# Kernel tuning notes

Hardware: AMD Instinct MI355X
Metric: run time of the kernel (lower is better)

## Reference

```python
import jax, jax.numpy as jnp
import numpy as np

EMBED_DIM = 1024
B, S = 4, 2048
SCALE = float(np.sqrt(EMBED_DIM))


def setup_inputs() -> dict:
    key = jax.random.key(0)
    ks = jax.random.split(key, 9)
    d = EMBED_DIM
    init = 1.0 / np.sqrt(d)
    return {
        "query": jax.random.normal(ks[0], (B, S, d), jnp.float32),
        "key": jax.random.normal(ks[1], (B, S, d), jnp.float32),
        "value": jax.random.normal(ks[2], (B, S, d), jnp.float32),
        "wq": jax.random.uniform(ks[3], (d, d), jnp.float32, -init, init),
        "bq": jax.random.uniform(ks[4], (d,), jnp.float32, -init, init),
        "wk": jax.random.uniform(ks[5], (d, d), jnp.float32, -init, init),
        "bk": jax.random.uniform(ks[6], (d,), jnp.float32, -init, init),
        "wv": jax.random.uniform(ks[7], (d, d), jnp.float32, -init, init),
        "bv": jax.random.uniform(ks[8], (d,), jnp.float32, -init, init),
    }


def reference(query, key, value, wq, bq, wk, bk, wv, bv):
    # Linear projections (torch Linear: x @ W^T + b; here weights stored as [in, out])
    q = query @ wq + bq            # [B,S,D]
    k = key @ wk + bk              # [B,S,D]
    v = value @ wv + bv            # [B,S,D]
    scores = jnp.einsum("bqd,bkd->bqk", q, k) / SCALE   # [B,S,S]
    attn = jax.nn.softmax(scores, axis=-1)
    # dropout in eval mode -> identity
    return jnp.einsum("bqk,bkd->bqd", attn, v)          # [B,S,D]
```

## Files before the change

kernel.cpp:

```cpp
#include <hip/hip_runtime.h>
#include <hip/hip_bf16.h>

typedef __attribute__((ext_vector_type(4))) float   f32x4;
typedef __attribute__((ext_vector_type(8))) __bf16  bf16x8;
typedef __attribute__((ext_vector_type(4))) __bf16  bf16x4;

#define NB 4
#define SS 2048
#define DD 1024

__device__ __forceinline__ void gload_lds16(const void* g, void* l) {
  __builtin_amdgcn_global_load_lds((const __attribute__((address_space(1))) void*)g,
                                   (__attribute__((address_space(3))) void*)l,
                                   16, 0, 0);
}

__global__ __launch_bounds__(256) void prep_kernel(
    const float* __restrict__ q, const float* __restrict__ k, const float* __restrict__ v,
    const float* __restrict__ wq, const float* __restrict__ wk, const float* __restrict__ wv,
    const float* __restrict__ bq, const float* __restrict__ bk, const float* __restrict__ bv,
    __bf16* __restrict__ X, __bf16* __restrict__ Wt, float* __restrict__ biasbuf)
{
  const int z = blockIdx.z;
  __shared__ float t[32][33];
  if (blockIdx.x < 8192) {
    const float* src = z == 0 ? q : (z == 1 ? k : v);
    __bf16* dst = X + (size_t)z * (size_t)(NB * SS * DD);
    size_t i = ((size_t)blockIdx.x * 256 + threadIdx.x) * 4;
    float4 f = *(const float4*)&src[i];
    bf16x4 o = { (__bf16)f.x, (__bf16)f.y, (__bf16)f.z, (__bf16)f.w };
    *(bf16x4*)&dst[i] = o;
  } else {
    const int idx = blockIdx.x - 8192;
    const float* W  = z == 0 ? wq : (z == 1 ? wk : wv);
    const float* bi = z == 0 ? bq : (z == 1 ? bk : bv);
    __bf16* dst = Wt + (size_t)z * (size_t)(DD * DD);
    const int n0 = (idx & 31) * 32, k0 = (idx >> 5) * 32;
    const int tx = threadIdx.x & 31, ty = threadIdx.x >> 5;
    #pragma unroll
    for (int i = 0; i < 4; i++)
      t[ty + 8 * i][tx] = W[(size_t)(k0 + ty + 8 * i) * DD + n0 + tx];
    __syncthreads();
    #pragma unroll
    for (int i = 0; i < 4; i++)
      dst[(size_t)(n0 + ty + 8 * i) * DD + k0 + tx] = (__bf16)t[tx][ty + 8 * i];
    if (idx == 0) {
      #pragma unroll
      for (int i = 0; i < 4; i++)
        biasbuf[z * DD + threadIdx.x + 256 * i] = bi[threadIdx.x + 256 * i];
    }
  }
}


#define G2A(BUF) ((BUF) * 16384)
#define G2B(BUF) (32768 + (BUF) * 16384)

#define G2_STAGE(BUF, T) do { int t_ = (((T) + koff) & (NT - 1));               \
  const __bf16* gA_ = Ablk + (size_t)t_ * 64;                                   \
  const __bf16* gB_ = Bblk + (size_t)t_ * 64;                                   \
  gload_lds16(gA_ + o0, smem + G2A(BUF) + tid * 16);                            \
  gload_lds16(gA_ + o1, smem + G2A(BUF) + 4096 + tid * 16);                     \
  gload_lds16(gA_ + o2, smem + G2A(BUF) + 8192 + tid * 16);                     \
  gload_lds16(gA_ + o3, smem + G2A(BUF) + 12288 + tid * 16);                    \
  gload_lds16(gB_ + o0, smem + G2B(BUF) + tid * 16);                            \
  gload_lds16(gB_ + o1, smem + G2B(BUF) + 4096 + tid * 16);                     \
  gload_lds16(gB_ + o2, smem + G2B(BUF) + 8192 + tid * 16);                     \
  gload_lds16(gB_ + o3, smem + G2B(BUF) + 12288 + tid * 16); } while (0)

template <int EPI>
__global__ __launch_bounds__(256, 2) void gemm2b_kernel(
    const __bf16* __restrict__ A, const __bf16* __restrict__ B,
    const float* __restrict__ bias, float* __restrict__ Fout,
    __bf16* __restrict__ Qo, __bf16* __restrict__ Ko, __bf16* __restrict__ Vt,
    int K, int lda, int ldb, int ldc,
    long strideA, long strideB, long strideC)
{
  extern __shared__ char smem[];

  const int gx = gridDim.x, gy = gridDim.y;
  const int nwg = gx * gy * gridDim.z;
  int lin = blockIdx.x + gx * (blockIdx.y + gy * blockIdx.z);
  const int cpx = nwg >> 3;
  int swz = (lin & 7) * cpx + (lin >> 3);
  const int bx = swz % gx;
  int rem = swz / gx;
  const int by = rem % gy;
  const int bz = rem / gy;

  const long brow = (long)by * 128, bcol = (long)bx * 128;
  const __bf16* Ablk = A + (size_t)bz * strideA + (size_t)brow * lda;
  const __bf16* Bblk = B + (size_t)bz * strideB + (size_t)bcol * ldb;

  const int tid  = threadIdx.x;
  const int lane = tid & 63;
  const int wid  = tid >> 6;
  const int wm = wid >> 1, wn = wid & 1;
  const int l15 = lane & 15, l4 = lane >> 4;
  const int lx = (lane & 7) << 4;

  const int NT = K >> 6;
  const int koff = (blockIdx.x & 1) * (NT >> 1);

  int o0, o1, o2, o3;
  #pragma unroll
  for (int i = 0; i < 4; ++i) {
    const int p = i * 4096 + tid * 16;
    const int r = p >> 7;
    const int kb = (p ^ ((r & 7) << 4)) & 127;
    const int off = r * lda + (kb >> 1);
    if (i == 0) o0 = off; else if (i == 1) o1 = off;
    else if (i == 2) o2 = off; else o3 = off;
  }

  int ara[2], brb[2];
  #pragma unroll
  for (int ks = 0; ks < 2; ++ks) {
    ara[ks] = ((((wm * 64 + l15) * 64 + l4 * 8) * 2) + ks * 64) ^ lx;
    brb[ks] = ((((wn * 64 + l15) * 64 + l4 * 8) * 2) + ks * 64) ^ lx;
  }

  f32x4 acc[4][4] = {};
  f32x4 accs[4] = {};
  bf16x8 af[4][2], bf[4][2];
  bf16x8 onesf;
  #pragma unroll
  for (int j = 0; j < 8; ++j) onesf[j] = (__bf16)1.0f;

  G2_STAGE(0, 0);
  G2_STAGE(1, 1);
  asm volatile("s_waitcnt vmcnt(8)" ::: "memory");
  __builtin_amdgcn_s_barrier();

  for (int t = 0; t < NT; ++t) {
    const int cur = t & 1;
    const int abase = cur * 16384;
    const int bbase = 32768 + cur * 16384;
    #pragma unroll
    for (int mi = 0; mi < 4; ++mi)
      #pragma unroll
      for (int ks = 0; ks < 2; ++ks)
        af[mi][ks] = *(const bf16x8*)(smem + abase + ara[ks] + mi * 2048);
    #pragma unroll
    for (int ni = 0; ni < 4; ++ni)
      #pragma unroll
      for (int ks = 0; ks < 2; ++ks)
        bf[ni][ks] = *(const bf16x8*)(smem + bbase + brb[ks] + ni * 2048);
    asm volatile("s_waitcnt lgkmcnt(0)" ::: "memory");
    __builtin_amdgcn_sched_barrier(0);
    __builtin_amdgcn_s_barrier();
    G2_STAGE(cur, t + 2);
    __builtin_amdgcn_s_setprio(1);
    #pragma unroll
    for (int mi = 0; mi < 4; ++mi)
      #pragma unroll
      for (int ni = 0; ni < 4; ++ni)
        #pragma unroll
        for (int ks = 0; ks < 2; ++ks)
          acc[mi][ni] = __builtin_amdgcn_mfma_f32_16x16x32_bf16(
              af[mi][ks], bf[ni][ks], acc[mi][ni], 0, 0, 0);
    if constexpr (EPI == 2) {
      #pragma unroll
      for (int mi = 0; mi < 4; ++mi)
        #pragma unroll
        for (int ks = 0; ks < 2; ++ks)
          accs[mi] = __builtin_amdgcn_mfma_f32_16x16x32_bf16(
              af[mi][ks], onesf, accs[mi], 0, 0, 0);
    }
    __builtin_amdgcn_s_setprio(0);
    __builtin_amdgcn_sched_barrier(0);
    asm volatile("s_waitcnt vmcnt(8)" ::: "memory");
    __builtin_amdgcn_s_barrier();
  }

  if constexpr (EPI == 2) {
    float* C = Fout + (size_t)bz * strideC;
    #pragma unroll
    for (int mi = 0; mi < 4; ++mi) {
      f32x4 inv;
      #pragma unroll
      for (int e = 0; e < 4; ++e) inv[e] = 1.0f / accs[mi][e];
      #pragma unroll
      for (int ni = 0; ni < 4; ++ni) {
        const long row = brow + wm * 64 + mi * 16 + l4 * 4;
        const long col = bcol + wn * 64 + ni * 16 + l15;
        #pragma unroll
        for (int e = 0; e < 4; ++e)
          C[(row + e) * (size_t)ldc + col] = acc[mi][ni][e] * inv[e];
      }
    }
  } else {
    if (bz == 2) {
      #pragma unroll
      for (int mi = 0; mi < 4; ++mi) {
        #pragma unroll
        for (int ni = 0; ni < 4; ++ni) {
          const long row = brow + wm * 64 + mi * 16 + l4 * 4;
          const long col = bcol + wn * 64 + ni * 16 + l15;
          const float bvv = bias[2 * DD + col];
          const long bb = row >> 11, s = row & 2047;
          bf16x4 pk = { (__bf16)(acc[mi][ni][0] + bvv), (__bf16)(acc[mi][ni][1] + bvv),
                        (__bf16)(acc[mi][ni][2] + bvv), (__bf16)(acc[mi][ni][3] + bvv) };
          *(bf16x4*)&Vt[bb * 2097152 + col * 2048 + s] = pk;
        }
      }
    } else {
      __bf16* C = bz == 0 ? Qo : Ko;
      #pragma unroll
      for (int mi = 0; mi < 4; ++mi) {
        #pragma unroll
        for (int ni = 0; ni < 4; ++ni) {
          const long row = brow + wm * 64 + mi * 16 + l4 * 4;
          const long col = bcol + wn * 64 + ni * 16 + l15;
          const float bvv = bias[bz * DD + col];
          #pragma unroll
          for (int e = 0; e < 4; ++e)
            C[(row + e) * 1024 + col] = (__bf16)(acc[mi][ni][e] + bvv);
        }
      }
    }
  }
}


#define A_OFF(BUF, MH) (((BUF)*2 + (MH)) * 16384)
#define B_OFF(BUF, NH) (65536 + ((BUF)*2 + (NH)) * 16384)

#define STAGE_A(BUF, MH, T) do { int t_ = (T); if (t_ >= NT) t_ = 0;            \
  const __bf16* gs_ = Ablk + (size_t)(MH) * (64 * (size_t)lda) + (size_t)t_ * 64; \
  gload_lds16(gs_ + aoff0, smem + A_OFF(BUF, MH) + tid * 16);                    \
  gload_lds16(gs_ + aoff1, smem + A_OFF(BUF, MH) + 8192 + tid * 16); } while (0)

#define STAGE_B(BUF, NH, T) do { int t_ = (T); if (t_ >= NT) t_ = 0;            \
  const __bf16* gs_ = Bblk + (size_t)(NH) * (32 * (size_t)ldb) + (size_t)t_ * 64; \
  gload_lds16(gs_ + boff0, smem + B_OFF(BUF, NH) + tid * 16);                    \
  gload_lds16(gs_ + boff1, smem + B_OFF(BUF, NH) + 8192 + tid * 16); } while (0)

#define DSREAD_A(DST, BUF, MH)                                                  \
  _Pragma("unroll") for (int mi = 0; mi < 4; ++mi) {                            \
    _Pragma("unroll") for (int ks = 0; ks < 2; ++ks)                            \
      DST[mi][ks] = *(const bf16x8*)(smem + A_OFF(BUF, MH) + arb[ks] + mi * 2048); }

#define DSREAD_BS(DST, BUF, NH)                                                 \
  _Pragma("unroll") for (int ni = 0; ni < 2; ++ni) {                            \
    _Pragma("unroll") for (int ks = 0; ks < 2; ++ks)                            \
      DST[ni][ks] = *(const bf16x8*)(smem + B_OFF(BUF, NH) + brb[ks] + ni * 2048); }

#define BARRIER_MFMA(AF, BF, MH, NH) do {                                       \
  __builtin_amdgcn_s_barrier();                                                 \
  asm volatile("s_waitcnt lgkmcnt(0)" ::: "memory");                            \
  __builtin_amdgcn_sched_barrier(0);                                            \
  __builtin_amdgcn_s_setprio(1);                                                \
  _Pragma("unroll") for (int mi = 0; mi < 4; ++mi)                              \
  _Pragma("unroll") for (int ni = 0; ni < 2; ++ni)                              \
  _Pragma("unroll") for (int ks = 0; ks < 2; ++ks)                              \
    acc[(MH)*4+mi][(NH)*2+ni] = __builtin_amdgcn_mfma_f32_16x16x32_bf16(        \
        AF[mi][ks], BF[ni][ks], acc[(MH)*4+mi][(NH)*2+ni], 0, 0, 0);            \
  __builtin_amdgcn_s_setprio(0);                                                \
  __builtin_amdgcn_sched_barrier(0);                                            \
  __builtin_amdgcn_s_barrier(); } while (0)

__global__ __launch_bounds__(512) void gemm8p_kernel(
    const __bf16* __restrict__ A, const __bf16* __restrict__ B,
    float scale, void* __restrict__ Cout,
    int K, int lda, int ldb, int ldc,
    long strideA, long strideB, long strideC)
{
  extern __shared__ char smem[];

  const int gx = gridDim.x, gy = gridDim.y;
  const int nwg = gx * gy * gridDim.z;
  int lin = blockIdx.x + gx * (blockIdx.y + gy * blockIdx.z);
  const int cpx = nwg >> 3;
  int swz = (lin & 7) * cpx + (lin >> 3);
  const int bx = swz % gx;
  int rem = swz / gx;
  const int by = rem % gy;
  const int bz = rem / gy;

  const long brow = (long)by * 256, bcol = (long)bx * 256;
  const __bf16* Ablk = A + (size_t)bz * strideA + (size_t)brow * lda;
  const __bf16* Bblk = B + (size_t)bz * strideB + (size_t)bcol * ldb;

  const int tid  = threadIdx.x;
  const int lane = tid & 63;
  const int wid  = tid >> 6;
  const int wm = wid >> 2, wn = wid & 3;
  const int l15 = lane & 15, l4 = lane >> 4;
  const int lx = (lane & 7) << 4;

  const int NT = K >> 6;
  const int niter = NT >> 1;

  int aoff0, aoff1, boff0, boff1;
  #pragma unroll
  for (int i = 0; i < 2; ++i) {
    const int p = i * 8192 + tid * 16;
    const int l = p ^ (((p >> 7) & 7) << 4);
    const int r = p >> 7;
    const int kb = l & 127;
    const int av = ((r >> 6) * 128 + (r & 63)) * lda + (kb >> 1);
    const int bv = ((r >> 5) * 64 + (r & 31)) * ldb + (kb >> 1);
    if (i == 0) { aoff0 = av; boff0 = bv; } else { aoff1 = av; boff1 = bv; }
  }

  int arb[2], brb[2];
  #pragma unroll
  for (int ks = 0; ks < 2; ++ks) {
    arb[ks] = ((((wm * 64 + l15) * 64 + l4 * 8) * 2) + ks * 64) ^ lx;
    brb[ks] = ((((wn * 32 + l15) * 64 + l4 * 8) * 2) + ks * 64) ^ lx;
  }

  f32x4 acc[8][4] = {};
  bf16x8 a0[4][2], a1[4][2], b0[2][2], b1[2][2];

  STAGE_B(0, 0, 0); STAGE_A(0, 0, 0); STAGE_A(0, 1, 0); STAGE_B(0, 1, 0);
  STAGE_B(1, 0, 1); STAGE_A(1, 0, 1);
  asm volatile("s_waitcnt vmcnt(4)" ::: "memory");
  __builtin_amdgcn_s_barrier();

  for (int it = 0; it < niter; ++it) {
    const int tt = it * 2;
    DSREAD_A(a0, 0, 0); DSREAD_BS(b0, 0, 0);
    STAGE_A(1, 1, tt + 1);
    BARRIER_MFMA(a0, b0, 0, 0);
    DSREAD_A(a1, 0, 1);
    STAGE_B(1, 1, tt + 1);
    BARRIER_MFMA(a1, b0, 1, 0);
    DSREAD_BS(b1, 0, 1);
    STAGE_B(0, 0, tt + 2);
    BARRIER_MFMA(a0, b1, 0, 1);
    STAGE_A(0, 0, tt + 2);
    asm volatile("s_waitcnt vmcnt(4)" ::: "memory");
    BARRIER_MFMA(a1, b1, 1, 1);
    DSREAD_A(a0, 1, 0); DSREAD_BS(b0, 1, 0);
    STAGE_A(0, 1, tt + 2);
    BARRIER_MFMA(a0, b0, 0, 0);
    DSREAD_A(a1, 1, 1);
    STAGE_B(0, 1, tt + 2);
    BARRIER_MFMA(a1, b0, 1, 0);
    DSREAD_BS(b1, 1, 1);
    STAGE_B(1, 0, tt + 3);
    BARRIER_MFMA(a0, b1, 0, 1);
    STAGE_A(1, 0, tt + 3);
    asm volatile("s_waitcnt vmcnt(4)" ::: "memory");
    BARRIER_MFMA(a1, b1, 1, 1);
  }

  const int cr = l4 * 4;
  __bf16* C = (__bf16*)Cout + (size_t)bz * strideC;
  #pragma unroll
  for (int m = 0; m < 8; ++m) {
    #pragma unroll
    for (int n = 0; n < 4; ++n) {
      const long row = brow + wm * 128 + m * 16 + cr;
      const long col = bcol + wn * 64 + n * 16 + l15;
      #pragma unroll
      for (int e = 0; e < 4; ++e)
        C[(row + e) * (size_t)ldc + col] = (__bf16)__expf(acc[m][n][e] * scale);
    }
  }
}

extern "C" void kernel_launch(void* const* d_in, const int* in_sizes, int n_in,
                              void* d_out, int out_size, void* d_ws, size_t ws_size,
                              hipStream_t stream)
{
  const float* query = (const float*)d_in[0];
  const float* key   = (const float*)d_in[1];
  const float* value = (const float*)d_in[2];
  const float* wq = (const float*)d_in[3];
  const float* bq = (const float*)d_in[4];
  const float* wk = (const float*)d_in[5];
  const float* bk = (const float*)d_in[6];
  const float* wv = (const float*)d_in[7];
  const float* bv = (const float*)d_in[8];

  char* ws = (char*)d_ws;
  __bf16* Xbf     = (__bf16*)(ws + 0);
  __bf16* Wt      = (__bf16*)(ws + 50331648);
  float*  biasbuf = (float*)(ws + 56623104);
  __bf16* Qb      = (__bf16*)(ws + 56635392);
  __bf16* Kb      = (__bf16*)(ws + 73412608);
  __bf16* Vt      = (__bf16*)(ws + 90189824);
  __bf16* P       = Xbf;

  hipFuncSetAttribute((const void*)gemm2b_kernel<0>, hipFuncAttributeMaxDynamicSharedMemorySize, 65536);
  hipFuncSetAttribute((const void*)gemm2b_kernel<2>, hipFuncAttributeMaxDynamicSharedMemorySize, 65536);
  hipFuncSetAttribute((const void*)gemm8p_kernel,    hipFuncAttributeMaxDynamicSharedMemorySize, 131072);

  dim3 b256(256), b512(512);

  prep_kernel<<<dim3(9216, 1, 3), b256, 0, stream>>>(
      query, key, value, wq, wk, wv, bq, bk, bv, Xbf, Wt, biasbuf);
  gemm2b_kernel<0><<<dim3(8, 64, 3), b256, 65536, stream>>>(
      Xbf, Wt, biasbuf, nullptr, Qb, Kb, Vt,
      1024, 1024, 1024, 1024,
      8388608L, 1048576L, 0L);
  gemm8p_kernel<<<dim3(8, 8, 4), b512, 131072, stream>>>(
      Qb, Kb, 0.03125f, P,
      1024, 1024, 1024, 2048,
      2097152L, 2097152L, 4194304L);
  gemm2b_kernel<2><<<dim3(8, 16, 4), b256, 65536, stream>>>(
      P, Vt, nullptr, (float*)d_out, nullptr, nullptr, nullptr,
      2048, 2048, 2048, 1024,
      4194304L, 2097152L, 2097152L);

  (void)in_sizes; (void)n_in; (void)out_size; (void)ws_size;
}
```

Measured before the change: 166.6 us.

## Compute softmax row sums in the scores kernel epilogue instead of via extra MFMAs

The P·V GEMM previously computed each row's softmax denominator by running extra MFMAs against a vector of ones inside its main loop. Now the QK^T kernel sums the bf16 exp values per row in its epilogue, using shuffles and an LDS reduction, and writes per-column-block partial sums to a workspace buffer. The P·V epilogue then reads the 8 partials per row and inverts their sum. This removes 8 MFMAs per K-step from the PV kernel. In exchange the scores kernel gets a reduction epilogue with an extra vmcnt wait and barriers.

```diff
diff --git a/kernel.cpp b/kernel.cpp
--- a/kernel.cpp
+++ b/kernel.cpp
@@ -71,7 +71,8 @@
 template <int EPI>
 __global__ __launch_bounds__(256, 2) void gemm2b_kernel(
     const __bf16* __restrict__ A, const __bf16* __restrict__ B,
-    const float* __restrict__ bias, float* __restrict__ Fout,
+    const float* __restrict__ bias, const float* __restrict__ rowpart,
+    float* __restrict__ Fout,
     __bf16* __restrict__ Qo, __bf16* __restrict__ Ko, __bf16* __restrict__ Vt,
     int K, int lda, int ldb, int ldc,
     long strideA, long strideB, long strideC)
@@ -121,11 +122,7 @@
   }
 
   f32x4 acc[4][4] = {};
-  f32x4 accs[4] = {};
   bf16x8 af[4][2], bf[4][2];
-  bf16x8 onesf;
-  #pragma unroll
-  for (int j = 0; j < 8; ++j) onesf[j] = (__bf16)1.0f;
 
   G2_STAGE(0, 0);
   G2_STAGE(1, 1);
@@ -159,14 +156,6 @@
         for (int ks = 0; ks < 2; ++ks)
           acc[mi][ni] = __builtin_amdgcn_mfma_f32_16x16x32_bf16(
               af[mi][ks], bf[ni][ks], acc[mi][ni], 0, 0, 0);
-    if constexpr (EPI == 2) {
-      #pragma unroll
-      for (int mi = 0; mi < 4; ++mi)
-        #pragma unroll
-        for (int ks = 0; ks < 2; ++ks)
-          accs[mi] = __builtin_amdgcn_mfma_f32_16x16x32_bf16(
-              af[mi][ks], onesf, accs[mi], 0, 0, 0);
-    }
     __builtin_amdgcn_s_setprio(0);
     __builtin_amdgcn_sched_barrier(0);
     asm volatile("s_waitcnt vmcnt(8)" ::: "memory");
@@ -179,7 +168,15 @@
     for (int mi = 0; mi < 4; ++mi) {
       f32x4 inv;
       #pragma unroll
-      for (int e = 0; e < 4; ++e) inv[e] = 1.0f / accs[mi][e];
+      for (int e = 0; e < 4; ++e) {
+        const long row = brow + wm * 64 + mi * 16 + l4 * 4 + e;
+        const size_t base = ((size_t)bz * 2048 + row) * 8;
+        const f32x4 r0 = *(const f32x4*)&rowpart[base];
+        const f32x4 r1 = *(const f32x4*)&rowpart[base + 4];
+        const float s = (r0[0] + r0[1] + r0[2] + r0[3]) +
+                        (r1[0] + r1[1] + r1[2] + r1[3]);
+        inv[e] = 1.0f / s;
+      }
       #pragma unroll
       for (int ni = 0; ni < 4; ++ni) {
         const long row = brow + wm * 64 + mi * 16 + l4 * 4;
@@ -262,7 +259,7 @@
 
 __global__ __launch_bounds__(512) void gemm8p_kernel(
     const __bf16* __restrict__ A, const __bf16* __restrict__ B,
-    float scale, void* __restrict__ Cout,
+    float scale, void* __restrict__ Cout, float* __restrict__ rowpart,
     int K, int lda, int ldb, int ldc,
     long strideA, long strideB, long strideC)
 {
@@ -349,6 +346,12 @@
 
   const int cr = l4 * 4;
   __bf16* C = (__bf16*)Cout + (size_t)bz * strideC;
+  float rsum[8][4];
+  #pragma unroll
+  for (int m = 0; m < 8; ++m)
+    #pragma unroll
+    for (int e = 0; e < 4; ++e) rsum[m][e] = 0.0f;
+
   #pragma unroll
   for (int m = 0; m < 8; ++m) {
     #pragma unroll
@@ -356,9 +359,38 @@
       const long row = brow + wm * 128 + m * 16 + cr;
       const long col = bcol + wn * 64 + n * 16 + l15;
       #pragma unroll
+      for (int e = 0; e < 4; ++e) {
+        const __bf16 v = (__bf16)__expf(acc[m][n][e] * scale);
+        C[(row + e) * (size_t)ldc + col] = v;
+        rsum[m][e] += (float)v;
+      }
+    }
+  }
+  #pragma unroll
+  for (int m = 0; m < 8; ++m)
+    #pragma unroll
+    for (int e = 0; e < 4; ++e)
+      #pragma unroll
+      for (int off = 1; off < 16; off <<= 1)
+        rsum[m][e] += __shfl_xor(rsum[m][e], off);
+
+  asm volatile("s_waitcnt vmcnt(0)" ::: "memory");
+  __builtin_amdgcn_s_barrier();
+  float* red = (float*)smem;
+  if (l15 == 0) {
+    #pragma unroll
+    for (int m = 0; m < 8; ++m)
+      #pragma unroll
       for (int e = 0; e < 4; ++e)
-        C[(row + e) * (size_t)ldc + col] = (__bf16)__expf(acc[m][n][e] * scale);
-    }
+        red[(wm * 4 + wn) * 128 + m * 16 + l4 * 4 + e] = rsum[m][e];
+  }
+  __builtin_amdgcn_s_barrier();
+  if (tid < 256) {
+    const int r = tid;
+    const int wmI = r >> 7, rI = r & 127;
+    const float s = red[(wmI * 4 + 0) * 128 + rI] + red[(wmI * 4 + 1) * 128 + rI] +
+                    red[(wmI * 4 + 2) * 128 + rI] + red[(wmI * 4 + 3) * 128 + rI];
+    rowpart[((size_t)bz * 2048 + brow + r) * 8 + bx] = s;
   }
 }
 
@@ -383,6 +415,7 @@
   __bf16* Qb      = (__bf16*)(ws + 56635392);
   __bf16* Kb      = (__bf16*)(ws + 73412608);
   __bf16* Vt      = (__bf16*)(ws + 90189824);
+  float*  rowpart = (float*)(ws + 106967040);
   __bf16* P       = Xbf;
 
   hipFuncSetAttribute((const void*)gemm2b_kernel<0>, hipFuncAttributeMaxDynamicSharedMemorySize, 65536);
@@ -394,15 +427,15 @@
   prep_kernel<<<dim3(9216, 1, 3), b256, 0, stream>>>(
       query, key, value, wq, wk, wv, bq, bk, bv, Xbf, Wt, biasbuf);
   gemm2b_kernel<0><<<dim3(8, 64, 3), b256, 65536, stream>>>(
-      Xbf, Wt, biasbuf, nullptr, Qb, Kb, Vt,
+      Xbf, Wt, biasbuf, nullptr, nullptr, Qb, Kb, Vt,
       1024, 1024, 1024, 1024,
       8388608L, 1048576L, 0L);
   gemm8p_kernel<<<dim3(8, 8, 4), b512, 131072, stream>>>(
-      Qb, Kb, 0.03125f, P,
+      Qb, Kb, 0.03125f, P, rowpart,
       1024, 1024, 1024, 2048,
       2097152L, 2097152L, 4194304L);
   gemm2b_kernel<2><<<dim3(8, 16, 4), b256, 65536, stream>>>(
-      P, Vt, nullptr, (float*)d_out, nullptr, nullptr, nullptr,
+      P, Vt, nullptr, rowpart, (float*)d_out, nullptr, nullptr, nullptr,
       2048, 2048, 2048, 1024,
       4194304L, 2097152L, 2097152L);
 
```

Measured after the change: 168.1 us. No clear change (+0.9%).
